# Optimization experiments

Hardware: AMD Instinct MI355X
Metric: run time of the kernel (lower is better)

Reference implementation:

```python
import jax, jax.numpy as jnp
import numpy as np

B = 1024
FEATS = [("sirna_gibbs_energy", 19), ("pssm_score", 1), ("gc_sterch", 1), ("sirna_second_percent", 2), ("sirna_second_energy", 2), ("tri_nt_percent", 64), ("di_nt_percent", 16), ("single_nt_percent", 4), ("gc_content", 1)]
DFF = 2048  # torch TransformerEncoderLayer default dim_feedforward


def _posenc(S, d):
    pos = jnp.arange(S, dtype=jnp.float32)[:, None]
    div = jnp.exp(jnp.arange(0, d, 2, dtype=jnp.float32) * (-np.log(10000.0) / d))
    pe = jnp.zeros((S, d), jnp.float32)
    pe = pe.at[:, 0::2].set(jnp.sin(pos * div))
    pe = pe.at[:, 1::2].set(jnp.cos(pos * div))
    return pe


def _ln(x, g, b):
    m = x.mean(-1, keepdims=True)
    v = ((x - m) ** 2).mean(-1, keepdims=True)
    return (x - m) * jax.lax.rsqrt(v + 1e-5) * g + b


def _encoder_layer(x, qkv_w, qkv_b, ow, ob, f1w, f1b, f2w, f2b, g1, b1, g2, b2, nhead):
    Bx, S, d = x.shape
    dh = d // nhead
    qkv = jnp.einsum('bsd,ed->bse', x, qkv_w) + qkv_b  # [B,S,3d]
    q, k, v = jnp.split(qkv, 3, axis=-1)
    sh = lambda t: t.reshape(Bx, S, nhead, dh).transpose(0, 2, 1, 3)  # [B,h,S,dh]
    q, k, v = sh(q), sh(k), sh(v)
    att = jax.nn.softmax(jnp.einsum('bhqd,bhkd->bhqk', q, k) / np.sqrt(dh).astype(np.float32), axis=-1)
    o = jnp.einsum('bhqk,bhkd->bhqd', att, v).transpose(0, 2, 1, 3).reshape(Bx, S, d)
    o = o @ ow.T + ob
    x = _ln(x + o, g1, b1)  # post-norm (norm_first=False default)
    h = jax.nn.relu(x @ f1w.T + f1b) @ f2w.T + f2b
    return _ln(x + h, g2, b2)


def _encoder(x, qkv_w, qkv_b, ow, ob, f1w, f1b, f2w, f2b, g1, b1, g2, b2, nhead):
    for i in range(qkv_w.shape[0]):
        x = _encoder_layer(x, qkv_w[i], qkv_b[i], ow[i], ob[i], f1w[i], f1b[i], f2w[i], f2b[i], g1[i], b1[i], g2[i], b2[i], nhead)
    return x


def setup_inputs():
    key = jax.random.key(0)
    ks = iter(jax.random.split(key, 128))
    inp = {}
    inp['rnafm_encode'] = jax.random.normal(next(ks), (B, 21, 640), jnp.float32)
    inp['rnafm_encode_mrna'] = jax.random.normal(next(ks), (B, 59, 640), jnp.float32)
    for name, n in FEATS:
        inp[name] = jax.random.normal(next(ks), (B, n, 1), jnp.float32)

    def xav(shape):
        fan_out, fan_in = shape[-2], shape[-1]
        std = np.sqrt(2.0 / (fan_in + fan_out)).astype(np.float32)
        return jax.random.normal(next(ks), shape, jnp.float32) * std

    def enc_params(prefix, L, d):
        inp[prefix + '_qkv_w'] = xav((L, 3 * d, d))
        inp[prefix + '_qkv_b'] = jnp.zeros((L, 3 * d), jnp.float32)
        inp[prefix + '_ow'] = xav((L, d, d))
        inp[prefix + '_ob'] = jnp.zeros((L, d), jnp.float32)
        inp[prefix + '_f1w'] = xav((L, DFF, d))
        inp[prefix + '_f1b'] = jnp.zeros((L, DFF), jnp.float32)
        inp[prefix + '_f2w'] = xav((L, d, DFF))
        inp[prefix + '_f2b'] = jnp.zeros((L, d), jnp.float32)
        inp[prefix + '_g1'] = jnp.ones((L, d), jnp.float32)
        inp[prefix + '_b1'] = jnp.zeros((L, d), jnp.float32)
        inp[prefix + '_g2'] = jnp.ones((L, d), jnp.float32)
        inp[prefix + '_b2'] = jnp.zeros((L, d), jnp.float32)

    inp['xmap1_w'] = xav((16, 640)); inp['xmap1_b'] = jnp.zeros(16, jnp.float32)
    enc_params('enc1', 4, 16)
    inp['ymap1_w'] = xav((4, 16)); inp['ymap1_b'] = jnp.zeros(4, jnp.float32)
    inp['xmap2_w'] = xav((8, 640)); inp['xmap2_b'] = jnp.zeros(8, jnp.float32)
    enc_params('enc2', 2, 8)
    inp['ymap2_w'] = xav((1, 8)); inp['ymap2_b'] = jnp.zeros(1, jnp.float32)
    inp['bn_g'] = jnp.ones(253, jnp.float32); inp['bn_b'] = jnp.zeros(253, jnp.float32)
    inp['d1w'] = xav((256, 253)); inp['d1b'] = jnp.zeros(256, jnp.float32)
    inp['d2w'] = xav((64, 256)); inp['d2b'] = jnp.zeros(64, jnp.float32)
    inp['d3w'] = xav((16, 64)); inp['d3b'] = jnp.zeros(16, jnp.float32)
    inp['d4w'] = xav((1, 16)); inp['d4b'] = jnp.zeros(1, jnp.float32)
    return inp


def _forward(rnafm_encode, rnafm_encode_mrna, feats,
             xmap1_w, xmap1_b, enc1, ymap1_w, ymap1_b,
             xmap2_w, xmap2_b, enc2, ymap2_w, ymap2_b,
             bn_g, bn_b, d1w, d1b, d2w, d2b, d3w, d3b, d4w, d4b):
    # siRNA branch: [B,21,640] -> [B,21,16] -> encoder(4 layers, 2 heads) -> [B,21,4]
    x = rnafm_encode @ xmap1_w.T + xmap1_b
    x = x + _posenc(21, 16)
    x = _encoder(x, *enc1, nhead=2)
    as_att = (x @ ymap1_w.T + ymap1_b).reshape(x.shape[0], -1)  # [B,84]
    # mRNA branch: [B,59,640] -> [B,59,8] -> encoder(2 layers, 1 head) -> [B,59,1]
    y = rnafm_encode_mrna @ xmap2_w.T + xmap2_b
    y = y + _posenc(59, 8)
    y = _encoder(y, *enc2, nhead=1)
    mrna_att = (y @ ymap2_w.T + ymap2_b).reshape(y.shape[0], -1)  # [B,59]
    other = jnp.concatenate([f[..., 0] for f in feats], axis=1)  # [B,110]
    cat = jnp.concatenate([as_att, mrna_att, other], axis=1)  # [B,253]
    # BatchNorm1d in eval mode (running_mean=0, running_var=1, eps=1e-5)
    h = cat * jax.lax.rsqrt(jnp.float32(1.0 + 1e-5)) * bn_g + bn_b
    h = jax.nn.leaky_relu(h @ d1w.T + d1b, 0.01)
    h = jax.nn.leaky_relu(h @ d2w.T + d2b, 0.01)
    h = jax.nn.leaky_relu(h @ d3w.T + d3b, 0.01)
    out = jax.nn.sigmoid(h @ d4w.T + d4b)
    return out[:, 0]


def reference(rnafm_encode, rnafm_encode_mrna, sirna_gibbs_energy, pssm_score, gc_sterch,
              sirna_second_percent, sirna_second_energy, tri_nt_percent, di_nt_percent,
              single_nt_percent, gc_content,
              xmap1_w, xmap1_b,
              enc1_qkv_w, enc1_qkv_b, enc1_ow, enc1_ob, enc1_f1w, enc1_f1b, enc1_f2w, enc1_f2b,
              enc1_g1, enc1_b1, enc1_g2, enc1_b2,
              ymap1_w, ymap1_b,
              xmap2_w, xmap2_b,
              enc2_qkv_w, enc2_qkv_b, enc2_ow, enc2_ob, enc2_f1w, enc2_f1b, enc2_f2w, enc2_f2b,
              enc2_g1, enc2_b1, enc2_g2, enc2_b2,
              ymap2_w, ymap2_b,
              bn_g, bn_b, d1w, d1b, d2w, d2b, d3w, d3b, d4w, d4b):
    feats = (sirna_gibbs_energy, pssm_score, gc_sterch, sirna_second_percent,
             sirna_second_energy, tri_nt_percent, di_nt_percent, single_nt_percent, gc_content)
    enc1 = (enc1_qkv_w, enc1_qkv_b, enc1_ow, enc1_ob, enc1_f1w, enc1_f1b, enc1_f2w, enc1_f2b,
            enc1_g1, enc1_b1, enc1_g2, enc1_b2)
    enc2 = (enc2_qkv_w, enc2_qkv_b, enc2_ow, enc2_ob, enc2_f1w, enc2_f1b, enc2_f2w, enc2_f2b,
            enc2_g1, enc2_b1, enc2_g2, enc2_b2)
    return _forward(rnafm_encode, rnafm_encode_mrna, feats,
                    xmap1_w, xmap1_b, enc1, ymap1_w, ymap1_b,
                    xmap2_w, xmap2_b, enc2, ymap2_w, ymap2_b,
                    bn_g, bn_b, d1w, d1b, d2w, d2b, d3w, d3b, d4w, d4b)
```

## Files before the change

### kernel.cpp

```cpp
#include <hip/hip_runtime.h>
#include <math.h>

#define NB 1024

typedef __bf16 mbf8 __attribute__((ext_vector_type(8)));
typedef float  mf4  __attribute__((ext_vector_type(4)));

union Pk { __bf16 h[4]; uint2 u2; };

__device__ __forceinline__ mf4 mfma16(mbf8 a, mbf8 b, mf4 c) {
  return __builtin_amdgcn_mfma_f32_16x16x32_bf16(a, b, c, 0, 0, 0);
}

__device__ __forceinline__ float dot4f(float4 a, float4 b){
  return a.x*b.x + a.y*b.y + a.z*b.z + a.w*b.w;
}

__device__ __forceinline__ mbf8 ld_frag_f32(const float* p) {
  float4 u0 = *(const float4*)p;
  float4 u1 = *(const float4*)(p + 4);
  mbf8 v;
  v[0]=(__bf16)u0.x; v[1]=(__bf16)u0.y; v[2]=(__bf16)u0.z; v[3]=(__bf16)u0.w;
  v[4]=(__bf16)u1.x; v[5]=(__bf16)u1.y; v[6]=(__bf16)u1.z; v[7]=(__bf16)u1.w;
  return v;
}

__device__ __forceinline__ mbf8 zero8() {
  mbf8 v;
  #pragma unroll
  for (int q = 0; q < 8; ++q) v[q] = (__bf16)0.f;
  return v;
}

__global__ __launch_bounds__(256) void prep_kernel(
    const float* __restrict__ xw1, const float* __restrict__ f1w1, const float* __restrict__ f2w1,
    const float* __restrict__ xw2, const float* __restrict__ f1w2, const float* __restrict__ f2w2,
    const float* __restrict__ d1w, const float* __restrict__ d2w, const float* __restrict__ d3w,
    __bf16* __restrict__ out)
{
  int idx = blockIdx.x * 256 + threadIdx.x;
  if (idx >= 693248) return;
  int which, local;
  if (idx < 10240)       { which = 0; local = idx; }
  else if (idx < 272384) { which = 1; local = idx - 10240; }
  else if (idx < 403456) { which = 2; local = idx - 272384; }
  else if (idx < 413696) { which = 3; local = idx - 403456; }
  else if (idx < 544768) { which = 4; local = idx - 413696; }
  else if (idx < 610304) { which = 5; local = idx - 544768; }
  else if (idx < 675840) { which = 6; local = idx - 610304; }
  else if (idx < 692224) { which = 7; local = idx - 675840; }
  else                   { which = 8; local = idx - 692224; }
  int tile = local >> 9, r = local & 511, lane = r >> 3, j = r & 7;
  int quad = lane >> 4, lm = lane & 15, khi = quad * 8 + j;
  float val = 0.f;
  switch (which) {
    case 0: { int k = tile*32 + khi; val = xw1[lm*640 + k]; } break;
    case 1: { int L = tile >> 7, nt = tile & 127, n = nt*16 + lm;
              val = (khi < 16) ? f1w1[(L*2048 + n)*16 + khi] : 0.f; } break;
    case 2: { int L = tile >> 6, ks = tile & 63, k = ks*32 + khi;
              val = f2w1[(L*16 + lm)*2048 + k]; } break;
    case 3: { int k = tile*32 + khi; val = (lm < 8) ? xw2[lm*640 + k] : 0.f; } break;
    case 4: { int L = tile >> 7, nt = tile & 127, n = nt*16 + lm;
              val = (khi < 8) ? f1w2[(L*2048 + n)*8 + khi] : 0.f; } break;
    case 5: { int L = tile >> 6, ks = tile & 63, k = ks*32 + khi;
              val = (lm < 8) ? f2w2[(L*8 + lm)*2048 + k] : 0.f; } break;
    case 6: { int nt = tile >> 3, ks = tile & 7, k = ks*32 + khi;
              val = (k < 253) ? d1w[(nt*16 + lm)*253 + k] : 0.f; } break;
    case 7: { int nt = tile >> 3, ks = tile & 7, k = ks*32 + khi;
              val = d2w[(nt*16 + lm)*256 + k]; } break;
    default:{ int ks = tile, k = ks*32 + khi;
              val = d3w[lm*64 + k]; } break;
  }
  out[idx] = (__bf16)val;
}

__device__ __forceinline__ void run_b1(int b, float* smem,
    const float* __restrict__ inp, const float* __restrict__ xb,
    const float* __restrict__ qw, const float* __restrict__ qb,
    const float* __restrict__ ow, const float* __restrict__ ob,
    const float* __restrict__ f1b, const float* __restrict__ f2b,
    const float* __restrict__ g1w, const float* __restrict__ b1w,
    const float* __restrict__ g2w, const float* __restrict__ b2w,
    const float* __restrict__ ymw, const float* __restrict__ ymb,
    const __bf16* __restrict__ xwB, const __bf16* __restrict__ w1B,
    const __bf16* __restrict__ w2B, float* __restrict__ outp)
{
  float* xs  = smem;
  float* xr  = smem + 420;
  float* ao  = smem + 840;
  float* pool= smem + 1264;
  float* mu  = smem + 5552;
  float* rsd = smem + 5573;

  const int tid = threadIdx.x;
  const int w = tid >> 6, lane = tid & 63, quad = lane >> 4, lm = lane & 15;
  float* qkv = pool;
  float* sc  = pool + 1092;
  float* red = pool;
  __bf16* hbuf = (__bf16*)pool;
  const float* Ain = inp + (size_t)b * 21 * 640;

  mf4 pc0 = {0.f,0.f,0.f,0.f}, pc1 = {0.f,0.f,0.f,0.f};
  for (int i = 0; i < 5; ++i) {
    int ks = w*5 + i;
    mbf8 bv = *(const mbf8*)(xwB + (ks*64 + lane)*8);
    #pragma unroll
    for (int mt = 0; mt < 2; ++mt) {
      int row = mt*16 + lm; row = row > 20 ? 20 : row;
      mbf8 av = ld_frag_f32(Ain + row*640 + ks*32 + quad*8);
      if (mt == 0) pc0 = mfma16(av, bv, pc0); else pc1 = mfma16(av, bv, pc1);
    }
  }
  #pragma unroll
  for (int r = 0; r < 4; ++r) {
    red[((w*2+0)*16 + quad*4 + r)*17 + lm] = pc0[r];
    red[((w*2+1)*16 + quad*4 + r)*17 + lm] = pc1[r];
  }
  __syncthreads();
  {
    const float lf = -logf(10000.0f) / 16.0f;
    for (int idx = tid; idx < 336; idx += 256) {
      int t = idx >> 4, i = idx & 15, mt = t >> 4, tl = t & 15;
      float s = red[((0+mt)*16+tl)*17+i] + red[((2+mt)*16+tl)*17+i]
              + red[((4+mt)*16+tl)*17+i] + red[((6+mt)*16+tl)*17+i];
      float freq = expf((float)((i>>1)*2) * lf);
      float pe = (i & 1) ? cosf((float)t * freq) : sinf((float)t * freq);
      xs[t*20 + i] = s + xb[i] + pe;
    }
  }
  __syncthreads();

  for (int L = 0; L < 4; ++L) {
    for (int idx = tid; idx < 1008; idx += 256) {
      int s = idx / 48, e = idx % 48;
      const float* wr = qw + (L*48 + e)*16;
      float a = qb[L*48 + e];
      #pragma unroll
      for (int k = 0; k < 16; ++k) a += xs[s*20+k] * wr[k];
      qkv[s*52 + e] = a;
    }
    __syncthreads();

    {
      int h = w >> 1, mt = w & 1;
      mbf8 qf = zero8();
      if (quad == 0) {
        int tok = mt*16 + lm; tok = tok > 20 ? 20 : tok;
        const float* p = qkv + tok*52 + h*8;
        #pragma unroll
        for (int j = 0; j < 8; ++j) qf[j] = (__bf16)(p[j] * 0.35355339059327373f);
      }
      #pragma unroll
      for (int nt = 0; nt < 2; ++nt) {
        mbf8 kf = zero8();
        if (quad == 0) {
          int key = nt*16 + lm; key = key > 20 ? 20 : key;
          const float* p = qkv + key*52 + 16 + h*8;
          #pragma unroll
          for (int j = 0; j < 8; ++j) kf[j] = (__bf16)p[j];
        }
        mf4 z = {0.f,0.f,0.f,0.f};
        mf4 c = mfma16(qf, kf, z);
        #pragma unroll
        for (int r = 0; r < 4; ++r) {
          int row = mt*16 + quad*4 + r, col = nt*16 + lm;
          if (row < 21 && col < 21) sc[(h*21 + row)*23 + col] = c[r];
        }
      }
    }
    __syncthreads();

    {
      int r = tid >> 2, p = tid & 3;
      if (r < 42) {
        float* row = sc + r*23;
        float m = -1e30f;
        for (int j = p; j < 21; j += 4) m = fmaxf(m, row[j]);
        m = fmaxf(m, __shfl_xor(m, 1));
        m = fmaxf(m, __shfl_xor(m, 2));
        float ssum = 0.f;
        for (int j = p; j < 21; j += 4) { float e = __expf(row[j] - m); row[j] = e; ssum += e; }
        ssum += __shfl_xor(ssum, 1);
        ssum += __shfl_xor(ssum, 2);
        float inv = 1.f / ssum;
        for (int j = p; j < 21; j += 4) row[j] *= inv;
      }
    }
    __syncthreads();

    {
      int h = w >> 1, mt = w & 1;
      mbf8 pf = zero8(), vf = zero8();
      {
        int tok = mt*16 + lm;
        #pragma unroll
        for (int j = 0; j < 8; ++j) {
          int k = quad*8 + j;
          pf[j] = (__bf16)((tok < 21 && k < 21) ? sc[(h*21 + tok)*23 + k] : 0.f);
          vf[j] = (__bf16)((lm < 8 && k < 21) ? qkv[k*52 + 32 + h*8 + lm] : 0.f);
        }
      }
      mf4 z = {0.f,0.f,0.f,0.f};
      mf4 c = mfma16(pf, vf, z);
      #pragma unroll
      for (int r = 0; r < 4; ++r) {
        int tok = mt*16 + quad*4 + r;
        if (tok < 21 && lm < 8) ao[tok*20 + h*8 + lm] = c[r];
      }
    }
    __syncthreads();

    for (int idx = tid; idx < 336; idx += 256) {
      int s = idx >> 4, i = idx & 15;
      const float* wr = ow + (L*16 + i)*16;
      float a = ob[L*16 + i];
      #pragma unroll
      for (int c = 0; c < 16; ++c) a += ao[s*20 + c] * wr[c];
      xr[s*20 + i] = xs[s*20 + i] + a;
    }
    __syncthreads();

    if (tid < 21) {
      float m = 0.f;
      #pragma unroll
      for (int k = 0; k < 16; ++k) m += xr[tid*20 + k];
      m *= (1.f/16.f);
      float v = 0.f;
      #pragma unroll
      for (int k = 0; k < 16; ++k) { float d = xr[tid*20 + k] - m; v += d*d; }
      v *= (1.f/16.f);
      mu[tid] = m; rsd[tid] = rsqrtf(v + 1e-5f);
    }
    __syncthreads();
    for (int idx = tid; idx < 336; idx += 256) {
      int s = idx >> 4, i = idx & 15;
      xs[s*20 + i] = (xr[s*20 + i] - mu[s]) * rsd[s] * g1w[L*16+i] + b1w[L*16+i];
    }
    __syncthreads();

    mbf8 xf0 = zero8(), xf1 = zero8();
    if (quad < 2) {
      int t0 = lm;
      int t1 = 16 + lm; if (t1 > 20) t1 = 20;
      xf0 = ld_frag_f32(xs + t0*20 + quad*8);
      xf1 = ld_frag_f32(xs + t1*20 + quad*8);
    }
    mf4 of0 = {0.f,0.f,0.f,0.f}, of1 = {0.f,0.f,0.f,0.f};
    const __bf16* w1L = w1B + (size_t)L*128*512;
    const __bf16* w2L = w2B + (size_t)L*64*512;
    const float* f1bL = f1b + L*2048;
    for (int ci = 0; ci < 8; ++ci) {
      #pragma unroll
      for (int u = 0; u < 4; ++u) {
        int ut = ci*16 + w*4 + u;
        mbf8 wa = *(const mbf8*)(w1L + (ut*64 + lane)*8);
        float4 bia = *(const float4*)(f1bL + ut*16 + quad*4);
        mf4 z = {0.f,0.f,0.f,0.f};
        mf4 c0 = mfma16(wa, xf0, z);
        mf4 c1 = mfma16(wa, xf1, z);
        Pk p0, p1;
        p0.h[0]=(__bf16)fmaxf(c0[0]+bia.x,0.f); p0.h[1]=(__bf16)fmaxf(c0[1]+bia.y,0.f);
        p0.h[2]=(__bf16)fmaxf(c0[2]+bia.z,0.f); p0.h[3]=(__bf16)fmaxf(c0[3]+bia.w,0.f);
        p1.h[0]=(__bf16)fmaxf(c1[0]+bia.x,0.f); p1.h[1]=(__bf16)fmaxf(c1[1]+bia.y,0.f);
        p1.h[2]=(__bf16)fmaxf(c1[2]+bia.z,0.f); p1.h[3]=(__bf16)fmaxf(c1[3]+bia.w,0.f);
        int colb = (ut & 15)*16 + quad*4;
        *(uint2*)(hbuf + lm*268 + colb)        = p0.u2;
        *(uint2*)(hbuf + (16 + lm)*268 + colb) = p1.u2;
      }
      #pragma unroll
      for (int kk = 0; kk < 2; ++kk) {
        int ksl = w*2 + kk;
        mbf8 wb = *(const mbf8*)(w2L + ((ci*8 + ksl)*64 + lane)*8);
        mbf8 a0 = *(const mbf8*)(hbuf + lm*268 + ksl*32 + quad*8);
        mbf8 a1 = *(const mbf8*)(hbuf + (16 + lm)*268 + ksl*32 + quad*8);
        of0 = mfma16(a0, wb, of0);
        of1 = mfma16(a1, wb, of1);
      }
    }
    __syncthreads();
    #pragma unroll
    for (int r = 0; r < 4; ++r) {
      red[((w*2+0)*16 + quad*4 + r)*17 + lm] = of0[r];
      red[((w*2+1)*16 + quad*4 + r)*17 + lm] = of1[r];
    }
    __syncthreads();
    for (int idx = tid; idx < 336; idx += 256) {
      int t = idx >> 4, i = idx & 15, mt = t >> 4, tl = t & 15;
      float s = red[((0+mt)*16+tl)*17+i] + red[((2+mt)*16+tl)*17+i]
              + red[((4+mt)*16+tl)*17+i] + red[((6+mt)*16+tl)*17+i];
      xr[t*20 + i] = xs[t*20 + i] + s + f2b[L*16 + i];
    }
    __syncthreads();
    if (tid < 21) {
      float m = 0.f;
      #pragma unroll
      for (int k = 0; k < 16; ++k) m += xr[tid*20 + k];
      m *= (1.f/16.f);
      float v = 0.f;
      #pragma unroll
      for (int k = 0; k < 16; ++k) { float d = xr[tid*20 + k] - m; v += d*d; }
      v *= (1.f/16.f);
      mu[tid] = m; rsd[tid] = rsqrtf(v + 1e-5f);
    }
    __syncthreads();
    for (int idx = tid; idx < 336; idx += 256) {
      int s = idx >> 4, i = idx & 15;
      xs[s*20 + i] = (xr[s*20 + i] - mu[s]) * rsd[s] * g2w[L*16+i] + b2w[L*16+i];
    }
    __syncthreads();
  }

  for (int idx = tid; idx < 84; idx += 256) {
    int s = idx >> 2, j = idx & 3;
    float a = ymb[j];
    #pragma unroll
    for (int k = 0; k < 16; ++k) a += xs[s*20 + k] * ymw[j*16 + k];
    outp[(size_t)b*84 + idx] = a;
  }
}

__device__ __forceinline__ void run_b2(int b, float* smem,
    const float* __restrict__ inp, const float* __restrict__ xb,
    const float* __restrict__ qw, const float* __restrict__ qb,
    const float* __restrict__ ow, const float* __restrict__ ob,
    const float* __restrict__ f1b, const float* __restrict__ f2b,
    const float* __restrict__ g1w, const float* __restrict__ b1w,
    const float* __restrict__ g2w, const float* __restrict__ b2w,
    const float* __restrict__ ymw, const float* __restrict__ ymb,
    const __bf16* __restrict__ xwB, const __bf16* __restrict__ w1B,
    const __bf16* __restrict__ w2B, float* __restrict__ outp)
{
  float* xs  = smem;
  float* xr  = smem + 708;
  float* ao  = smem + 1416;
  float* pool= smem + 2124;
  float* mu  = smem + 7375;
  float* rsd = smem + 7434;

  const int tid = threadIdx.x;
  const int w = tid >> 6, lane = tid & 63, quad = lane >> 4, lm = lane & 15;
  float* qkv = pool;
  float* sc  = pool + 1652;
  float* red = pool;
  __bf16* hbuf = (__bf16*)pool;
  const float* Ain = inp + (size_t)b * 59 * 640;

  mf4 pc[4];
  #pragma unroll
  for (int mt = 0; mt < 4; ++mt) { mf4 z = {0.f,0.f,0.f,0.f}; pc[mt] = z; }
  for (int i = 0; i < 5; ++i) {
    int ks = w*5 + i;
    mbf8 bv = *(const mbf8*)(xwB + (ks*64 + lane)*8);
    #pragma unroll
    for (int mt = 0; mt < 4; ++mt) {
      int row = mt*16 + lm; row = row > 58 ? 58 : row;
      mbf8 av = ld_frag_f32(Ain + row*640 + ks*32 + quad*8);
      pc[mt] = mfma16(av, bv, pc[mt]);
    }
  }
  #pragma unroll
  for (int mt = 0; mt < 4; ++mt)
    #pragma unroll
    for (int r = 0; r < 4; ++r)
      red[((w*4+mt)*16 + quad*4 + r)*17 + lm] = pc[mt][r];
  __syncthreads();
  {
    const float lf = -logf(10000.0f) / 8.0f;
    for (int idx = tid; idx < 472; idx += 256) {
      int t = idx >> 3, i = idx & 7, mt = t >> 4, tl = t & 15;
      float s = red[((0*4+mt)*16+tl)*17+i] + red[((1*4+mt)*16+tl)*17+i]
              + red[((2*4+mt)*16+tl)*17+i] + red[((3*4+mt)*16+tl)*17+i];
      float freq = expf((float)((i>>1)*2) * lf);
      float pe = (i & 1) ? cosf((float)t * freq) : sinf((float)t * freq);
      xs[t*12 + i] = s + xb[i] + pe;
    }
  }
  __syncthreads();

  for (int L = 0; L < 2; ++L) {
    for (int idx = tid; idx < 1416; idx += 256) {
      int s = idx / 24, e = idx % 24;
      const float* wr = qw + (L*24 + e)*8;
      float a = qb[L*24 + e];
      #pragma unroll
      for (int k = 0; k < 8; ++k) a += xs[s*12+k] * wr[k];
      qkv[s*28 + e] = a;
    }
    __syncthreads();

    {
      mbf8 qf = zero8();
      if (quad == 0) {
        int tok = w*16 + lm; tok = tok > 58 ? 58 : tok;
        const float* p = qkv + tok*28;
        #pragma unroll
        for (int j = 0; j < 8; ++j) qf[j] = (__bf16)(p[j] * 0.35355339059327373f);
      }
      #pragma unroll
      for (int nt = 0; nt < 4; ++nt) {
        mbf8 kf = zero8();
        if (quad == 0) {
          int key = nt*16 + lm; key = key > 58 ? 58 : key;
          const float* p = qkv + key*28 + 8;
          #pragma unroll
          for (int j = 0; j < 8; ++j) kf[j] = (__bf16)p[j];
        }
        mf4 z = {0.f,0.f,0.f,0.f};
        mf4 c = mfma16(qf, kf, z);
        #pragma unroll
        for (int r = 0; r < 4; ++r) {
          int row = w*16 + quad*4 + r, col = nt*16 + lm;
          if (row < 59 && col < 59) sc[row*61 + col] = c[r];
        }
      }
    }
    __syncthreads();

    {
      int r = tid >> 2, p = tid & 3;
      if (r < 59) {
        float* row = sc + r*61;
        float m = -1e30f;
        for (int j = p; j < 59; j += 4) m = fmaxf(m, row[j]);
        m = fmaxf(m, __shfl_xor(m, 1));
        m = fmaxf(m, __shfl_xor(m, 2));
        float ssum = 0.f;
        for (int j = p; j < 59; j += 4) { float e = __expf(row[j] - m); row[j] = e; ssum += e; }
        ssum += __shfl_xor(ssum, 1);
        ssum += __shfl_xor(ssum, 2);
        float inv = 1.f / ssum;
        for (int j = p; j < 59; j += 4) row[j] *= inv;
      }
    }
    __syncthreads();

    {
      mf4 acc = {0.f,0.f,0.f,0.f};
      #pragma unroll
      for (int kk = 0; kk < 2; ++kk) {
        mbf8 pf = zero8(), vf = zero8();
        int tok = w*16 + lm;
        #pragma unroll
        for (int j = 0; j < 8; ++j) {
          int k = kk*32 + quad*8 + j;
          pf[j] = (__bf16)((tok < 59 && k < 59) ? sc[tok*61 + k] : 0.f);
          vf[j] = (__bf16)((lm < 8 && k < 59) ? qkv[k*28 + 16 + lm] : 0.f);
        }
        acc = mfma16(pf, vf, acc);
      }
      #pragma unroll
      for (int r = 0; r < 4; ++r) {
        int tok = w*16 + quad*4 + r;
        if (tok < 59 && lm < 8) ao[tok*12 + lm] = acc[r];
      }
    }
    __syncthreads();

    for (int idx = tid; idx < 472; idx += 256) {
      int s = idx >> 3, i = idx & 7;
      const float* wr = ow + (L*8 + i)*8;
      float a = ob[L*8 + i];
      #pragma unroll
      for (int c = 0; c < 8; ++c) a += ao[s*12 + c] * wr[c];
      xr[s*12 + i] = xs[s*12 + i] + a;
    }
    __syncthreads();

    if (tid < 59) {
      float m = 0.f;
      #pragma unroll
      for (int k = 0; k < 8; ++k) m += xr[tid*12 + k];
      m *= 0.125f;
      float v = 0.f;
      #pragma unroll
      for (int k = 0; k < 8; ++k) { float d = xr[tid*12 + k] - m; v += d*d; }
      v *= 0.125f;
      mu[tid] = m; rsd[tid] = rsqrtf(v + 1e-5f);
    }
    __syncthreads();
    for (int idx = tid; idx < 472; idx += 256) {
      int s = idx >> 3, i = idx & 7;
      xs[s*12 + i] = (xr[s*12 + i] - mu[s]) * rsd[s] * g1w[L*8+i] + b1w[L*8+i];
    }
    __syncthreads();

    mbf8 xf[4];
    #pragma unroll
    for (int tt = 0; tt < 4; ++tt) {
      xf[tt] = zero8();
      if (quad == 0) {
        int tok = tt*16 + lm; if (tok > 58) tok = 58;
        xf[tt] = ld_frag_f32(xs + tok*12);
      }
    }
    mf4 of[4];
    #pragma unroll
    for (int mt = 0; mt < 4; ++mt) { mf4 z = {0.f,0.f,0.f,0.f}; of[mt] = z; }
    const __bf16* w1L = w1B + (size_t)L*128*512;
    const __bf16* w2L = w2B + (size_t)L*64*512;
    const float* f1bL = f1b + L*2048;
    for (int ci = 0; ci < 16; ++ci) {
      #pragma unroll
      for (int u = 0; u < 2; ++u) {
        int ut = ci*8 + w*2 + u;
        mbf8 wa = *(const mbf8*)(w1L + (ut*64 + lane)*8);
        float4 bia = *(const float4*)(f1bL + ut*16 + quad*4);
        int colb = (ut & 7)*16 + quad*4;
        #pragma unroll
        for (int tt = 0; tt < 4; ++tt) {
          mf4 z = {0.f,0.f,0.f,0.f};
          mf4 c = mfma16(wa, xf[tt], z);
          Pk p;
          p.h[0]=(__bf16)fmaxf(c[0]+bia.x,0.f); p.h[1]=(__bf16)fmaxf(c[1]+bia.y,0.f);
          p.h[2]=(__bf16)fmaxf(c[2]+bia.z,0.f); p.h[3]=(__bf16)fmaxf(c[3]+bia.w,0.f);
          *(uint2*)(hbuf + (tt*16 + lm)*140 + colb) = p.u2;
        }
      }
      {
        mbf8 wb = *(const mbf8*)(w2L + ((ci*4 + w)*64 + lane)*8);
        #pragma unroll
        for (int mt = 0; mt < 4; ++mt) {
          mbf8 ah = *(const mbf8*)(hbuf + (mt*16 + lm)*140 + w*32 + quad*8);
          of[mt] = mfma16(ah, wb, of[mt]);
        }
      }
    }
    __syncthreads();
    #pragma unroll
    for (int mt = 0; mt < 4; ++mt)
      #pragma unroll
      for (int r = 0; r < 4; ++r)
        red[((w*4+mt)*16 + quad*4 + r)*17 + lm] = of[mt][r];
    __syncthreads();
    for (int idx = tid; idx < 472; idx += 256) {
      int t = idx >> 3, i = idx & 7, mt = t >> 4, tl = t & 15;
      float s = red[((0*4+mt)*16+tl)*17+i] + red[((1*4+mt)*16+tl)*17+i]
              + red[((2*4+mt)*16+tl)*17+i] + red[((3*4+mt)*16+tl)*17+i];
      xr[t*12 + i] = xs[t*12 + i] + s + f2b[L*8 + i];
    }
    __syncthreads();
    if (tid < 59) {
      float m = 0.f;
      #pragma unroll
      for (int k = 0; k < 8; ++k) m += xr[tid*12 + k];
      m *= 0.125f;
      float v = 0.f;
      #pragma unroll
      for (int k = 0; k < 8; ++k) { float d = xr[tid*12 + k] - m; v += d*d; }
      v *= 0.125f;
      mu[tid] = m; rsd[tid] = rsqrtf(v + 1e-5f);
    }
    __syncthreads();
    for (int idx = tid; idx < 472; idx += 256) {
      int s = idx >> 3, i = idx & 7;
      xs[s*12 + i] = (xr[s*12 + i] - mu[s]) * rsd[s] * g2w[L*8+i] + b2w[L*8+i];
    }
    __syncthreads();
  }

  for (int s = tid; s < 59; s += 256) {
    float a = ymb[0];
    #pragma unroll
    for (int k = 0; k < 8; ++k) a += xs[s*12 + k] * ymw[k];
    outp[(size_t)b*59 + s] = a;
  }
}

__global__ __launch_bounds__(256) void enc_kernel(
    const float* __restrict__ inp1, const float* __restrict__ inp2,
    const float* __restrict__ xb1,
    const float* __restrict__ qw1, const float* __restrict__ qb1,
    const float* __restrict__ ow1, const float* __restrict__ ob1,
    const float* __restrict__ f1b1, const float* __restrict__ f2b1,
    const float* __restrict__ g1w1, const float* __restrict__ b1w1,
    const float* __restrict__ g2w1, const float* __restrict__ b2w1,
    const float* __restrict__ ymw1, const float* __restrict__ ymb1,
    const __bf16* __restrict__ xw1B, const __bf16* __restrict__ w1B1,
    const __bf16* __restrict__ w2B1,
    const float* __restrict__ xb2,
    const float* __restrict__ qw2, const float* __restrict__ qb2,
    const float* __restrict__ ow2, const float* __restrict__ ob2,
    const float* __restrict__ f1b2, const float* __restrict__ f2b2,
    const float* __restrict__ g1w2, const float* __restrict__ b1w2,
    const float* __restrict__ g2w2, const float* __restrict__ b2w2,
    const float* __restrict__ ymw2, const float* __restrict__ ymb2,
    const __bf16* __restrict__ xw2B, const __bf16* __restrict__ w1B2,
    const __bf16* __restrict__ w2B2,
    float* __restrict__ as_att, float* __restrict__ mrna)
{
  __shared__ __align__(16) float smem[7600];
  int bid = blockIdx.x;
  int b = bid >> 1;
  if ((bid & 1) == 0) {
    run_b1(b, smem, inp1, xb1, qw1, qb1, ow1, ob1, f1b1, f2b1,
           g1w1, b1w1, g2w1, b2w1, ymw1, ymb1, xw1B, w1B1, w2B1, as_att);
  } else {
    run_b2(b, smem, inp2, xb2, qw2, qb2, ow2, ob2, f1b2, f2b2,
           g1w2, b1w2, g2w2, b2w2, ymw2, ymb2, xw2B, w1B2, w2B2, mrna);
  }
}

__global__ __launch_bounds__(256) void mlp_kernel(
    const float* __restrict__ as_att, const float* __restrict__ mrna,
    const float* __restrict__ f_gibbs, const float* __restrict__ f_pssm,
    const float* __restrict__ f_gcs, const float* __restrict__ f_ssp,
    const float* __restrict__ f_sse, const float* __restrict__ f_tri,
    const float* __restrict__ f_di, const float* __restrict__ f_sgl,
    const float* __restrict__ f_gc,
    const float* __restrict__ bn_g, const float* __restrict__ bn_b,
    const float* __restrict__ d1b, const float* __restrict__ d2b,
    const float* __restrict__ d3b,
    const float* __restrict__ d4w, const float* __restrict__ d4b,
    const __bf16* __restrict__ d1B, const __bf16* __restrict__ d2B,
    const __bf16* __restrict__ d3B,
    float* __restrict__ outp)
{
  __shared__ __align__(16) float cat[16*268];
  __shared__ __align__(16) float h1[16*268];
  __shared__ __align__(16) float h2[16*68];
  __shared__ __align__(16) float h3[16*17];
  const int tid = threadIdx.x;
  const int bs  = blockIdx.x * 16;
  const int w = tid >> 6, lane = tid & 63, quad = lane >> 4, lm = lane & 15;
  const float bnscale = rsqrtf(1.0f + 1e-5f);

  for (int g = 0; g < 16; ++g) {
    int smp = bs + g;
    for (int j = tid; j < 253; j += 256) {
      float v;
      if (j < 84)       v = as_att[(size_t)smp*84 + j];
      else if (j < 143) v = mrna[(size_t)smp*59 + (j - 84)];
      else {
        int j2 = j - 143;
        if (j2 < 19)       v = f_gibbs[smp*19 + j2];
        else if (j2 < 20)  v = f_pssm[smp];
        else if (j2 < 21)  v = f_gcs[smp];
        else if (j2 < 23)  v = f_ssp[smp*2 + (j2-21)];
        else if (j2 < 25)  v = f_sse[smp*2 + (j2-23)];
        else if (j2 < 89)  v = f_tri[smp*64 + (j2-25)];
        else if (j2 < 105) v = f_di[smp*16 + (j2-89)];
        else if (j2 < 109) v = f_sgl[smp*4 + (j2-105)];
        else               v = f_gc[smp];
      }
      cat[g*268 + j] = v * bnscale * bn_g[j] + bn_b[j];
    }
  }
  if (tid < 48) { int g = tid / 3; cat[g*268 + 253 + tid % 3] = 0.f; }
  __syncthreads();

  {
    mf4 acc[4];
    #pragma unroll
    for (int q = 0; q < 4; ++q) { mf4 z = {0.f,0.f,0.f,0.f}; acc[q] = z; }
    for (int ks = 0; ks < 8; ++ks) {
      mbf8 af = ld_frag_f32(cat + lm*268 + ks*32 + quad*8);
      #pragma unroll
      for (int nt4 = 0; nt4 < 4; ++nt4) {
        int nt = w*4 + nt4;
        mbf8 bf = *(const mbf8*)(d1B + ((nt*8 + ks)*64 + lane)*8);
        acc[nt4] = mfma16(af, bf, acc[nt4]);
      }
    }
    #pragma unroll
    for (int nt4 = 0; nt4 < 4; ++nt4) {
      int n = (w*4 + nt4)*16 + lm;
      float bb = d1b[n];
      #pragma unroll
      for (int r = 0; r < 4; ++r) {
        float a = acc[nt4][r] + bb;
        h1[(quad*4 + r)*268 + n] = (a > 0.f) ? a : 0.01f * a;
      }
    }
  }
  __syncthreads();

  {
    mf4 acc = {0.f,0.f,0.f,0.f};
    for (int ks = 0; ks < 8; ++ks) {
      mbf8 af = ld_frag_f32(h1 + lm*268 + ks*32 + quad*8);
      mbf8 bf = *(const mbf8*)(d2B + ((w*8 + ks)*64 + lane)*8);
      acc = mfma16(af, bf, acc);
    }
    int n = w*16 + lm;
    float bb = d2b[n];
    #pragma unroll
    for (int r = 0; r < 4; ++r) {
      float a = acc[r] + bb;
      h2[(quad*4 + r)*68 + n] = (a > 0.f) ? a : 0.01f * a;
    }
  }
  __syncthreads();

  if (w == 0) {
    mf4 acc = {0.f,0.f,0.f,0.f};
    #pragma unroll
    for (int ks = 0; ks < 2; ++ks) {
      mbf8 af = ld_frag_f32(h2 + lm*68 + ks*32 + quad*8);
      mbf8 bf = *(const mbf8*)(d3B + (ks*64 + lane)*8);
      acc = mfma16(af, bf, acc);
    }
    float bb = d3b[lm];
    #pragma unroll
    for (int r = 0; r < 4; ++r) {
      float a = acc[r] + bb;
      h3[(quad*4 + r)*17 + lm] = (a > 0.f) ? a : 0.01f * a;
    }
  }
  __syncthreads();

  if (tid < 16) {
    float a = d4b[0];
    #pragma unroll
    for (int j = 0; j < 16; ++j) a += h3[tid*17 + j] * d4w[j];
    outp[bs + tid] = 1.f / (1.f + __expf(-a));
  }
}

extern "C" void kernel_launch(void* const* d_in, const int* in_sizes, int n_in,
                              void* d_out, int out_size, void* d_ws, size_t ws_size,
                              hipStream_t stream) {
  const float* rnafm   = (const float*)d_in[0];
  const float* rnafm_m = (const float*)d_in[1];
  const float* f_gibbs = (const float*)d_in[2];
  const float* f_pssm  = (const float*)d_in[3];
  const float* f_gcs   = (const float*)d_in[4];
  const float* f_ssp   = (const float*)d_in[5];
  const float* f_sse   = (const float*)d_in[6];
  const float* f_tri   = (const float*)d_in[7];
  const float* f_di    = (const float*)d_in[8];
  const float* f_sgl   = (const float*)d_in[9];
  const float* f_gc    = (const float*)d_in[10];
  const float* xmap1_w = (const float*)d_in[11];
  const float* xmap1_b = (const float*)d_in[12];
  const float* e1_qw   = (const float*)d_in[13];
  const float* e1_qb   = (const float*)d_in[14];
  const float* e1_ow   = (const float*)d_in[15];
  const float* e1_ob   = (const float*)d_in[16];
  const float* e1_f1w  = (const float*)d_in[17];
  const float* e1_f1b  = (const float*)d_in[18];
  const float* e1_f2w  = (const float*)d_in[19];
  const float* e1_f2b  = (const float*)d_in[20];
  const float* e1_g1   = (const float*)d_in[21];
  const float* e1_b1   = (const float*)d_in[22];
  const float* e1_g2   = (const float*)d_in[23];
  const float* e1_b2   = (const float*)d_in[24];
  const float* ymap1_w = (const float*)d_in[25];
  const float* ymap1_b = (const float*)d_in[26];
  const float* xmap2_w = (const float*)d_in[27];
  const float* xmap2_b = (const float*)d_in[28];
  const float* e2_qw   = (const float*)d_in[29];
  const float* e2_qb   = (const float*)d_in[30];
  const float* e2_ow   = (const float*)d_in[31];
  const float* e2_ob   = (const float*)d_in[32];
  const float* e2_f1w  = (const float*)d_in[33];
  const float* e2_f1b  = (const float*)d_in[34];
  const float* e2_f2w  = (const float*)d_in[35];
  const float* e2_f2b  = (const float*)d_in[36];
  const float* e2_g1   = (const float*)d_in[37];
  const float* e2_b1   = (const float*)d_in[38];
  const float* e2_g2   = (const float*)d_in[39];
  const float* e2_b2   = (const float*)d_in[40];
  const float* ymap2_w = (const float*)d_in[41];
  const float* ymap2_b = (const float*)d_in[42];
  const float* bn_g    = (const float*)d_in[43];
  const float* bn_b    = (const float*)d_in[44];
  const float* d1w     = (const float*)d_in[45];
  const float* d1b     = (const float*)d_in[46];
  const float* d2w     = (const float*)d_in[47];
  const float* d2b     = (const float*)d_in[48];
  const float* d3w     = (const float*)d_in[49];
  const float* d3b     = (const float*)d_in[50];
  const float* d4w     = (const float*)d_in[51];
  const float* d4b     = (const float*)d_in[52];

  float* as_att = (float*)d_ws;
  float* mrna   = (float*)((char*)d_ws + (size_t)NB*84*4);
  __bf16* bfb   = (__bf16*)((char*)d_ws + 585728);
  __bf16* xw1B  = bfb;
  __bf16* w1B1  = bfb + 10240;
  __bf16* w2B1  = bfb + 272384;
  __bf16* xw2B  = bfb + 403456;
  __bf16* w1B2  = bfb + 413696;
  __bf16* w2B2  = bfb + 544768;
  __bf16* d1B   = bfb + 610304;
  __bf16* d2B   = bfb + 675840;
  __bf16* d3B   = bfb + 692224;
  float* outp   = (float*)d_out;

  prep_kernel<<<2708, 256, 0, stream>>>(xmap1_w, e1_f1w, e1_f2w, xmap2_w, e2_f1w, e2_f2w,
                                        d1w, d2w, d3w, bfb);

  enc_kernel<<<2*NB, 256, 0, stream>>>(rnafm, rnafm_m,
      xmap1_b, e1_qw, e1_qb, e1_ow, e1_ob, e1_f1b, e1_f2b,
      e1_g1, e1_b1, e1_g2, e1_b2, ymap1_w, ymap1_b, xw1B, w1B1, w2B1,
      xmap2_b, e2_qw, e2_qb, e2_ow, e2_ob, e2_f1b, e2_f2b,
      e2_g1, e2_b1, e2_g2, e2_b2, ymap2_w, ymap2_b, xw2B, w1B2, w2B2,
      as_att, mrna);

  mlp_kernel<<<64, 256, 0, stream>>>(as_att, mrna,
      f_gibbs, f_pssm, f_gcs, f_ssp, f_sse, f_tri, f_di, f_sgl, f_gc,
      bn_g, bn_b, d1b, d2b, d3b, d4w, d4b, d1B, d2B, d3B, outp);
}
```

Measured before the change: 593.5 us.

## Fuse softmax and layernorm into registers, drop barriers, shrink shared memory

```diff
diff --git a/kernel.cpp b/kernel.cpp
--- a/kernel.cpp
+++ b/kernel.cpp
@@ -10,10 +10,6 @@
 
 __device__ __forceinline__ mf4 mfma16(mbf8 a, mbf8 b, mf4 c) {
   return __builtin_amdgcn_mfma_f32_16x16x32_bf16(a, b, c, 0, 0, 0);
-}
-
-__device__ __forceinline__ float dot4f(float4 a, float4 b){
-  return a.x*b.x + a.y*b.y + a.z*b.z + a.w*b.w;
 }
 
 __device__ __forceinline__ mbf8 ld_frag_f32(const float* p) {
@@ -22,6 +18,15 @@
   mbf8 v;
   v[0]=(__bf16)u0.x; v[1]=(__bf16)u0.y; v[2]=(__bf16)u0.z; v[3]=(__bf16)u0.w;
   v[4]=(__bf16)u1.x; v[5]=(__bf16)u1.y; v[6]=(__bf16)u1.z; v[7]=(__bf16)u1.w;
+  return v;
+}
+
+__device__ __forceinline__ mbf8 ld_frag_f32_scaled(const float* p, float s) {
+  float4 u0 = *(const float4*)p;
+  float4 u1 = *(const float4*)(p + 4);
+  mbf8 v;
+  v[0]=(__bf16)(u0.x*s); v[1]=(__bf16)(u0.y*s); v[2]=(__bf16)(u0.z*s); v[3]=(__bf16)(u0.w*s);
+  v[4]=(__bf16)(u1.x*s); v[5]=(__bf16)(u1.y*s); v[6]=(__bf16)(u1.z*s); v[7]=(__bf16)(u1.w*s);
   return v;
 }
 
@@ -85,19 +90,16 @@
     const __bf16* __restrict__ xwB, const __bf16* __restrict__ w1B,
     const __bf16* __restrict__ w2B, float* __restrict__ outp)
 {
-  float* xs  = smem;
-  float* xr  = smem + 420;
-  float* ao  = smem + 840;
-  float* pool= smem + 1264;
-  float* mu  = smem + 5552;
-  float* rsd = smem + 5573;
+  float* xs   = smem;
+  float* ao   = smem + 420;
+  float* pool = smem + 840;
 
   const int tid = threadIdx.x;
   const int w = tid >> 6, lane = tid & 63, quad = lane >> 4, lm = lane & 15;
   float* qkv = pool;
-  float* sc  = pool + 1092;
+  __bf16* pbuf = (__bf16*)(pool + 1092);
+  __bf16* hbuf = (__bf16*)pool;
   float* red = pool;
-  __bf16* hbuf = (__bf16*)pool;
   const float* Ain = inp + (size_t)b * 21 * 640;
 
   mf4 pc0 = {0.f,0.f,0.f,0.f}, pc1 = {0.f,0.f,0.f,0.f};
@@ -143,62 +145,45 @@
 
     {
       int h = w >> 1, mt = w & 1;
+      __bf16* pb = pbuf + w*640;
+      int tokq = mt*16 + lm; tokq = tokq > 20 ? 20 : tokq;
       mbf8 qf = zero8();
-      if (quad == 0) {
-        int tok = mt*16 + lm; tok = tok > 20 ? 20 : tok;
-        const float* p = qkv + tok*52 + h*8;
-        #pragma unroll
-        for (int j = 0; j < 8; ++j) qf[j] = (__bf16)(p[j] * 0.35355339059327373f);
-      }
+      if (quad == 0) qf = ld_frag_f32_scaled(qkv + tokq*52 + h*8, 0.35355339059327373f);
+      float scr[2][4];
       #pragma unroll
       for (int nt = 0; nt < 2; ++nt) {
+        int key = nt*16 + lm; key = key > 20 ? 20 : key;
         mbf8 kf = zero8();
-        if (quad == 0) {
-          int key = nt*16 + lm; key = key > 20 ? 20 : key;
-          const float* p = qkv + key*52 + 16 + h*8;
-          #pragma unroll
-          for (int j = 0; j < 8; ++j) kf[j] = (__bf16)p[j];
-        }
+        if (quad == 0) kf = ld_frag_f32(qkv + key*52 + 16 + h*8);
         mf4 z = {0.f,0.f,0.f,0.f};
         mf4 c = mfma16(qf, kf, z);
+        int col = nt*16 + lm;
         #pragma unroll
-        for (int r = 0; r < 4; ++r) {
-          int row = mt*16 + quad*4 + r, col = nt*16 + lm;
-          if (row < 21 && col < 21) sc[(h*21 + row)*23 + col] = c[r];
-        }
-      }
-    }
-    __syncthreads();
-
-    {
-      int r = tid >> 2, p = tid & 3;
-      if (r < 42) {
-        float* row = sc + r*23;
-        float m = -1e30f;
-        for (int j = p; j < 21; j += 4) m = fmaxf(m, row[j]);
-        m = fmaxf(m, __shfl_xor(m, 1));
-        m = fmaxf(m, __shfl_xor(m, 2));
-        float ssum = 0.f;
-        for (int j = p; j < 21; j += 4) { float e = __expf(row[j] - m); row[j] = e; ssum += e; }
-        ssum += __shfl_xor(ssum, 1);
-        ssum += __shfl_xor(ssum, 2);
-        float inv = 1.f / ssum;
-        for (int j = p; j < 21; j += 4) row[j] *= inv;
-      }
-    }
-    __syncthreads();
-
-    {
-      int h = w >> 1, mt = w & 1;
-      mbf8 pf = zero8(), vf = zero8();
-      {
-        int tok = mt*16 + lm;
+        for (int r = 0; r < 4; ++r) scr[nt][r] = (col < 21) ? c[r] : -1e30f;
+      }
+      #pragma unroll
+      for (int r = 0; r < 4; ++r) {
+        float m = fmaxf(scr[0][r], scr[1][r]);
+        m = fmaxf(m, __shfl_xor(m, 1)); m = fmaxf(m, __shfl_xor(m, 2));
+        m = fmaxf(m, __shfl_xor(m, 4)); m = fmaxf(m, __shfl_xor(m, 8));
+        float e0 = __expf(scr[0][r] - m), e1 = __expf(scr[1][r] - m);
+        float s = e0 + e1;
+        s += __shfl_xor(s, 1); s += __shfl_xor(s, 2);
+        s += __shfl_xor(s, 4); s += __shfl_xor(s, 8);
+        float inv = 1.f / s;
+        scr[0][r] = e0 * inv; scr[1][r] = e1 * inv;
+      }
+      #pragma unroll
+      for (int nt = 0; nt < 2; ++nt)
         #pragma unroll
-        for (int j = 0; j < 8; ++j) {
-          int k = quad*8 + j;
-          pf[j] = (__bf16)((tok < 21 && k < 21) ? sc[(h*21 + tok)*23 + k] : 0.f);
-          vf[j] = (__bf16)((lm < 8 && k < 21) ? qkv[k*52 + 32 + h*8 + lm] : 0.f);
-        }
+        for (int r = 0; r < 4; ++r)
+          pb[(quad*4 + r)*40 + nt*16 + lm] = (__bf16)scr[nt][r];
+      mbf8 pf = *(const mbf8*)(pb + lm*40 + quad*8);
+      mbf8 vf = zero8();
+      #pragma unroll
+      for (int j = 0; j < 8; ++j) {
+        int k = quad*8 + j;
+        vf[j] = (__bf16)((lm < 8 && k < 21) ? qkv[k*52 + 32 + h*8 + lm] : 0.f);
       }
       mf4 z = {0.f,0.f,0.f,0.f};
       mf4 c = mfma16(pf, vf, z);
@@ -216,25 +201,17 @@
       float a = ob[L*16 + i];
       #pragma unroll
       for (int c = 0; c < 16; ++c) a += ao[s*20 + c] * wr[c];
-      xr[s*20 + i] = xs[s*20 + i] + a;
-    }
-    __syncthreads();
-
-    if (tid < 21) {
-      float m = 0.f;
-      #pragma unroll
-      for (int k = 0; k < 16; ++k) m += xr[tid*20 + k];
+      float v = xs[s*20 + i] + a;
+      float m = v;
+      m += __shfl_xor(m, 1); m += __shfl_xor(m, 2);
+      m += __shfl_xor(m, 4); m += __shfl_xor(m, 8);
       m *= (1.f/16.f);
-      float v = 0.f;
-      #pragma unroll
-      for (int k = 0; k < 16; ++k) { float d = xr[tid*20 + k] - m; v += d*d; }
-      v *= (1.f/16.f);
-      mu[tid] = m; rsd[tid] = rsqrtf(v + 1e-5f);
-    }
-    __syncthreads();
-    for (int idx = tid; idx < 336; idx += 256) {
-      int s = idx >> 4, i = idx & 15;
-      xs[s*20 + i] = (xr[s*20 + i] - mu[s]) * rsd[s] * g1w[L*16+i] + b1w[L*16+i];
+      float d = v - m;
+      float va = d*d;
+      va += __shfl_xor(va, 1); va += __shfl_xor(va, 2);
+      va += __shfl_xor(va, 4); va += __shfl_xor(va, 8);
+      va *= (1.f/16.f);
+      xs[s*20 + i] = d * rsqrtf(va + 1e-5f) * g1w[L*16+i] + b1w[L*16+i];
     }
     __syncthreads();
 
@@ -264,15 +241,15 @@
         p1.h[0]=(__bf16)fmaxf(c1[0]+bia.x,0.f); p1.h[1]=(__bf16)fmaxf(c1[1]+bia.y,0.f);
         p1.h[2]=(__bf16)fmaxf(c1[2]+bia.z,0.f); p1.h[3]=(__bf16)fmaxf(c1[3]+bia.w,0.f);
         int colb = (ut & 15)*16 + quad*4;
-        *(uint2*)(hbuf + lm*268 + colb)        = p0.u2;
-        *(uint2*)(hbuf + (16 + lm)*268 + colb) = p1.u2;
+        *(uint2*)(hbuf + lm*264 + colb)        = p0.u2;
+        *(uint2*)(hbuf + (16 + lm)*264 + colb) = p1.u2;
       }
       #pragma unroll
       for (int kk = 0; kk < 2; ++kk) {
         int ksl = w*2 + kk;
         mbf8 wb = *(const mbf8*)(w2L + ((ci*8 + ksl)*64 + lane)*8);
-        mbf8 a0 = *(const mbf8*)(hbuf + lm*268 + ksl*32 + quad*8);
-        mbf8 a1 = *(const mbf8*)(hbuf + (16 + lm)*268 + ksl*32 + quad*8);
+        mbf8 a0 = *(const mbf8*)(hbuf + lm*264 + ksl*32 + quad*8);
+        mbf8 a1 = *(const mbf8*)(hbuf + (16 + lm)*264 + ksl*32 + quad*8);
         of0 = mfma16(a0, wb, of0);
         of1 = mfma16(a1, wb, of1);
       }
@@ -288,24 +265,17 @@
       int t = idx >> 4, i = idx & 15, mt = t >> 4, tl = t & 15;
       float s = red[((0+mt)*16+tl)*17+i] + red[((2+mt)*16+tl)*17+i]
               + red[((4+mt)*16+tl)*17+i] + red[((6+mt)*16+tl)*17+i];
-      xr[t*20 + i] = xs[t*20 + i] + s + f2b[L*16 + i];
-    }
-    __syncthreads();
-    if (tid < 21) {
-      float m = 0.f;
-      #pragma unroll
-      for (int k = 0; k < 16; ++k) m += xr[tid*20 + k];
+      float v = xs[t*20 + i] + s + f2b[L*16 + i];
+      float m = v;
+      m += __shfl_xor(m, 1); m += __shfl_xor(m, 2);
+      m += __shfl_xor(m, 4); m += __shfl_xor(m, 8);
       m *= (1.f/16.f);
-      float v = 0.f;
-      #pragma unroll
-      for (int k = 0; k < 16; ++k) { float d = xr[tid*20 + k] - m; v += d*d; }
-      v *= (1.f/16.f);
-      mu[tid] = m; rsd[tid] = rsqrtf(v + 1e-5f);
-    }
-    __syncthreads();
-    for (int idx = tid; idx < 336; idx += 256) {
-      int s = idx >> 4, i = idx & 15;
-      xs[s*20 + i] = (xr[s*20 + i] - mu[s]) * rsd[s] * g2w[L*16+i] + b2w[L*16+i];
+      float d = v - m;
+      float va = d*d;
+      va += __shfl_xor(va, 1); va += __shfl_xor(va, 2);
+      va += __shfl_xor(va, 4); va += __shfl_xor(va, 8);
+      va *= (1.f/16.f);
+      xs[t*20 + i] = d * rsqrtf(va + 1e-5f) * g2w[L*16+i] + b2w[L*16+i];
     }
     __syncthreads();
   }
@@ -330,19 +300,16 @@
     const __bf16* __restrict__ xwB, const __bf16* __restrict__ w1B,
     const __bf16* __restrict__ w2B, float* __restrict__ outp)
 {
-  float* xs  = smem;
-  float* xr  = smem + 708;
-  float* ao  = smem + 1416;
-  float* pool= smem + 2124;
-  float* mu  = smem + 7375;
-  float* rsd = smem + 7434;
+  float* xs   = smem;
+  float* ao   = smem + 708;
+  float* pool = smem + 1416;
 
   const int tid = threadIdx.x;
   const int w = tid >> 6, lane = tid & 63, quad = lane >> 4, lm = lane & 15;
   float* qkv = pool;
-  float* sc  = pool + 1652;
+  __bf16* pbuf = (__bf16*)(pool + 1652);
+  __bf16* hbuf = (__bf16*)pool;
   float* red = pool;
-  __bf16* hbuf = (__bf16*)pool;
   const float* Ain = inp + (size_t)b * 59 * 640;
 
   mf4 pc[4];
@@ -389,61 +356,49 @@
     __syncthreads();
 
     {
+      __bf16* pb = pbuf + w*1152;
+      int tokq = w*16 + lm; tokq = tokq > 58 ? 58 : tokq;
       mbf8 qf = zero8();
-      if (quad == 0) {
-        int tok = w*16 + lm; tok = tok > 58 ? 58 : tok;
-        const float* p = qkv + tok*28;
-        #pragma unroll
-        for (int j = 0; j < 8; ++j) qf[j] = (__bf16)(p[j] * 0.35355339059327373f);
-      }
+      if (quad == 0) qf = ld_frag_f32_scaled(qkv + tokq*28, 0.35355339059327373f);
+      float scr[4][4];
       #pragma unroll
       for (int nt = 0; nt < 4; ++nt) {
+        int key = nt*16 + lm; key = key > 58 ? 58 : key;
         mbf8 kf = zero8();
-        if (quad == 0) {
-          int key = nt*16 + lm; key = key > 58 ? 58 : key;
-          const float* p = qkv + key*28 + 8;
-          #pragma unroll
-          for (int j = 0; j < 8; ++j) kf[j] = (__bf16)p[j];
-        }
+        if (quad == 0) kf = ld_frag_f32(qkv + key*28 + 8);
         mf4 z = {0.f,0.f,0.f,0.f};
         mf4 c = mfma16(qf, kf, z);
+        int col = nt*16 + lm;
         #pragma unroll
-        for (int r = 0; r < 4; ++r) {
-          int row = w*16 + quad*4 + r, col = nt*16 + lm;
-          if (row < 59 && col < 59) sc[row*61 + col] = c[r];
-        }
-      }
-    }
-    __syncthreads();
-
-    {
-      int r = tid >> 2, p = tid & 3;
-      if (r < 59) {
-        float* row = sc + r*61;
-        float m = -1e30f;
-        for (int j = p; j < 59; j += 4) m = fmaxf(m, row[j]);
-        m = fmaxf(m, __shfl_xor(m, 1));
-        m = fmaxf(m, __shfl_xor(m, 2));
-        float ssum = 0.f;
-        for (int j = p; j < 59; j += 4) { float e = __expf(row[j] - m); row[j] = e; ssum += e; }
-        ssum += __shfl_xor(ssum, 1);
-        ssum += __shfl_xor(ssum, 2);
-        float inv = 1.f / ssum;
-        for (int j = p; j < 59; j += 4) row[j] *= inv;
-      }
-    }
-    __syncthreads();
-
-    {
+        for (int r = 0; r < 4; ++r) scr[nt][r] = (col < 59) ? c[r] : -1e30f;
+      }
+      #pragma unroll
+      for (int r = 0; r < 4; ++r) {
+        float m = fmaxf(fmaxf(scr[0][r], scr[1][r]), fmaxf(scr[2][r], scr[3][r]));
+        m = fmaxf(m, __shfl_xor(m, 1)); m = fmaxf(m, __shfl_xor(m, 2));
+        m = fmaxf(m, __shfl_xor(m, 4)); m = fmaxf(m, __shfl_xor(m, 8));
+        float e0 = __expf(scr[0][r] - m), e1 = __expf(scr[1][r] - m);
+        float e2 = __expf(scr[2][r] - m), e3 = __expf(scr[3][r] - m);
+        float s = (e0 + e1) + (e2 + e3);
+        s += __shfl_xor(s, 1); s += __shfl_xor(s, 2);
+        s += __shfl_xor(s, 4); s += __shfl_xor(s, 8);
+        float inv = 1.f / s;
+        scr[0][r] = e0 * inv; scr[1][r] = e1 * inv;
+        scr[2][r] = e2 * inv; scr[3][r] = e3 * inv;
+      }
+      #pragma unroll
+      for (int nt = 0; nt < 4; ++nt)
+        #pragma unroll
+        for (int r = 0; r < 4; ++r)
+          pb[(quad*4 + r)*72 + nt*16 + lm] = (__bf16)scr[nt][r];
       mf4 acc = {0.f,0.f,0.f,0.f};
       #pragma unroll
       for (int kk = 0; kk < 2; ++kk) {
-        mbf8 pf = zero8(), vf = zero8();
-        int tok = w*16 + lm;
+        mbf8 pf = *(const mbf8*)(pb + lm*72 + kk*32 + quad*8);
+        mbf8 vf = zero8();
         #pragma unroll
         for (int j = 0; j < 8; ++j) {
           int k = kk*32 + quad*8 + j;
-          pf[j] = (__bf16)((tok < 59 && k < 59) ? sc[tok*61 + k] : 0.f);
           vf[j] = (__bf16)((lm < 8 && k < 59) ? qkv[k*28 + 16 + lm] : 0.f);
         }
         acc = mfma16(pf, vf, acc);
@@ -462,25 +417,15 @@
       float a = ob[L*8 + i];
       #pragma unroll
       for (int c = 0; c < 8; ++c) a += ao[s*12 + c] * wr[c];
-      xr[s*12 + i] = xs[s*12 + i] + a;
-    }
-    __syncthreads();
-
-    if (tid < 59) {
-      float m = 0.f;
-      #pragma unroll
-      for (int k = 0; k < 8; ++k) m += xr[tid*12 + k];
+      float v = xs[s*12 + i] + a;
+      float m = v;
+      m += __shfl_xor(m, 1); m += __shfl_xor(m, 2); m += __shfl_xor(m, 4);
       m *= 0.125f;
-      float v = 0.f;
-      #pragma unroll
-      for (int k = 0; k < 8; ++k) { float d = xr[tid*12 + k] - m; v += d*d; }
-      v *= 0.125f;
-      mu[tid] = m; rsd[tid] = rsqrtf(v + 1e-5f);
-    }
-    __syncthreads();
-    for (int idx = tid; idx < 472; idx += 256) {
-      int s = idx >> 3, i = idx & 7;
-      xs[s*12 + i] = (xr[s*12 + i] - mu[s]) * rsd[s] * g1w[L*8+i] + b1w[L*8+i];
+      float d = v - m;
+      float va = d*d;
+      va += __shfl_xor(va, 1); va += __shfl_xor(va, 2); va += __shfl_xor(va, 4);
+      va *= 0.125f;
+      xs[s*12 + i] = d * rsqrtf(va + 1e-5f) * g1w[L*8+i] + b1w[L*8+i];
     }
     __syncthreads();
 
@@ -513,14 +458,14 @@
           Pk p;
           p.h[0]=(__bf16)fmaxf(c[0]+bia.x,0.f); p.h[1]=(__bf16)fmaxf(c[1]+bia.y,0.f);
           p.h[2]=(__bf16)fmaxf(c[2]+bia.z,0.f); p.h[3]=(__bf16)fmaxf(c[3]+bia.w,0.f);
-          *(uint2*)(hbuf + (tt*16 + lm)*140 + colb) = p.u2;
+          *(uint2*)(hbuf + (tt*16 + lm)*136 + colb) = p.u2;
         }
       }
       {
         mbf8 wb = *(const mbf8*)(w2L + ((ci*4 + w)*64 + lane)*8);
         #pragma unroll
         for (int mt = 0; mt < 4; ++mt) {
-          mbf8 ah = *(const mbf8*)(hbuf + (mt*16 + lm)*140 + w*32 + quad*8);
+          mbf8 ah = *(const mbf8*)(hbuf + (mt*16 + lm)*136 + w*32 + quad*8);
           of[mt] = mfma16(ah, wb, of[mt]);
         }
       }
@@ -536,24 +481,15 @@
       int t = idx >> 3, i = idx & 7, mt = t >> 4, tl = t & 15;
       float s = red[((0*4+mt)*16+tl)*17+i] + red[((1*4+mt)*16+tl)*17+i]
               + red[((2*4+mt)*16+tl)*17+i] + red[((3*4+mt)*16+tl)*17+i];
-      xr[t*12 + i] = xs[t*12 + i] + s + f2b[L*8 + i];
-    }
-    __syncthreads();
-    if (tid < 59) {
-      float m = 0.f;
-      #pragma unroll
-      for (int k = 0; k < 8; ++k) m += xr[tid*12 + k];
+      float v = xs[t*12 + i] + s + f2b[L*8 + i];
+      float m = v;
+      m += __shfl_xor(m, 1); m += __shfl_xor(m, 2); m += __shfl_xor(m, 4);
       m *= 0.125f;
-      float v = 0.f;
-      #pragma unroll
-      for (int k = 0; k < 8; ++k) { float d = xr[tid*12 + k] - m; v += d*d; }
-      v *= 0.125f;
-      mu[tid] = m; rsd[tid] = rsqrtf(v + 1e-5f);
-    }
-    __syncthreads();
-    for (int idx = tid; idx < 472; idx += 256) {
-      int s = idx >> 3, i = idx & 7;
-      xs[s*12 + i] = (xr[s*12 + i] - mu[s]) * rsd[s] * g2w[L*8+i] + b2w[L*8+i];
+      float d = v - m;
+      float va = d*d;
+      va += __shfl_xor(va, 1); va += __shfl_xor(va, 2); va += __shfl_xor(va, 4);
+      va *= 0.125f;
+      xs[t*12 + i] = d * rsqrtf(va + 1e-5f) * g2w[L*8+i] + b2w[L*8+i];
     }
     __syncthreads();
   }
@@ -588,7 +524,7 @@
     const __bf16* __restrict__ w2B2,
     float* __restrict__ as_att, float* __restrict__ mrna)
 {
-  __shared__ __align__(16) float smem[7600];
+  __shared__ __align__(16) float smem[5792];
   int bid = blockIdx.x;
   int b = bid >> 1;
   if ((bid & 1) == 0) {
```

Result: faster. 516.6 us (-13.0%).
